# Kernel tuning notes

Hardware: AMD Instinct MI355X
Metric: run time of the kernel (lower is better)

## Reference

```python
import jax, jax.numpy as jnp
import numpy as np

B = 32           # graphs in batch
N_PER = 512      # nodes per graph
N = B * N_PER    # 16384 total nodes (block-diagonal batched graph)
E = N * 16       # 262144 edges
D_IN = 128
D_OUT = 128
ASSIGN = 2048    # total clusters = B * K
K = ASSIGN // B  # 64 clusters per graph


def setup_inputs() -> dict:
    key = jax.random.key(0)
    ks = jax.random.split(key, 6)
    h = jax.random.normal(ks[0], (N, D_IN), jnp.float32)
    # edges confined within each graph -> block-diagonal batched adjacency
    gid = jnp.repeat(jnp.arange(B), E // B)
    edge_src = (jax.random.randint(ks[1], (E,), 0, N_PER) + gid * N_PER).astype(jnp.int32)
    edge_dst = (jax.random.randint(ks[2], (E,), 0, N_PER) + gid * N_PER).astype(jnp.int32)
    # GraphSage NodeApply linears: Linear(2*in, out)
    stdv_f = 1.0 / np.sqrt(2 * D_IN)
    W_feat = jax.random.uniform(ks[3], (2 * D_IN, D_OUT), jnp.float32, -stdv_f, stdv_f)
    b_feat = jnp.zeros((D_OUT,), jnp.float32)
    W_pool = jax.random.uniform(ks[4], (2 * D_IN, ASSIGN), jnp.float32, -stdv_f, stdv_f)
    b_pool = jnp.zeros((ASSIGN,), jnp.float32)
    return {"h": h, "W_feat": W_feat, "b_feat": b_feat,
            "W_pool": W_pool, "b_pool": b_pool,
            "edge_src": edge_src, "edge_dst": edge_dst}


def _graphsage(h, W, b, src, dst):
    # mean aggregation over in-neighbors (dropout=0, batch_norm off)
    msg = jax.ops.segment_sum(h[src], dst, num_segments=N)          # [N, d_in]
    deg = jax.ops.segment_sum(jnp.ones((src.shape[0],), h.dtype), dst, num_segments=N)
    h_neigh = msg / jnp.maximum(deg, 1.0)[:, None]
    bundle = jnp.concatenate([h, h_neigh], axis=1) @ W + b          # [N, d_out]
    # F.normalize(p=2, dim=1) then activation, as in GraphSage NodeApply
    norm = jnp.linalg.norm(bundle, axis=1, keepdims=True)
    bundle = bundle / jnp.maximum(norm, 1e-12)
    return jax.nn.relu(bundle)


def _forward(h, W_feat, b_feat, W_pool, b_pool, src, dst):
    feat = _graphsage(h, W_feat, b_feat, src, dst)       # [N, D_OUT]
    assign = _graphsage(h, W_pool, b_pool, src, dst)     # [N, ASSIGN]
    # block-diagonal mask: node i of graph g may only assign to g's K clusters
    gid_n = jnp.arange(N) // N_PER                       # [N]
    gid_c = jnp.arange(ASSIGN) // K                      # [ASSIGN]
    mask = (gid_n[:, None] == gid_c[None, :]).astype(jnp.float32)
    # masked_softmax with memory_efficient=False
    s = jax.nn.softmax(assign * mask, axis=-1) * mask
    s = s / (s.sum(axis=-1, keepdims=True) + 1e-13)      # [N, ASSIGN]
    h_new = s.T @ feat                                   # [ASSIGN, D_OUT]
    # adj_new = S^T A S without densifying A: (A S)[dst] += S[src]
    a_s = jax.ops.segment_sum(s[src], dst, num_segments=N)
    adj_new = s.T @ a_s                                  # [ASSIGN, ASSIGN]
    return adj_new, h_new


def reference(h, W_feat, b_feat, W_pool, b_pool, edge_src, edge_dst):
    return _forward(h, W_feat, b_feat, W_pool, b_pool, edge_src, edge_dst)
```

## Files before the change

### kernel.cpp

```cpp
#include <hip/hip_runtime.h>

#define NB   32
#define NPER 512
#define NN   16384
#define EE   262144
#define DD   128
#define AS   2048
#define KC   64

using short8   = __attribute__((ext_vector_type(8))) short;
using floatx4  = __attribute__((ext_vector_type(4))) float;
using ushort4v = __attribute__((ext_vector_type(4))) unsigned short;

typedef __attribute__((address_space(3))) unsigned int lds_u32;
typedef const __attribute__((address_space(1))) unsigned int gbl_u32;

static __device__ __forceinline__ void gload16(const unsigned short* g, unsigned short* l) {
    __builtin_amdgcn_global_load_lds((gbl_u32*)g, (lds_u32*)l, 16, 0, 0);
}

static __device__ __forceinline__ float bits2f(unsigned int u) {
    union { unsigned int i; float f; } z; z.i = u << 16; return z.f;
}
static __device__ __forceinline__ unsigned short f2b(float x) {
    union { float f; unsigned int u; } v; v.f = x;
    unsigned int r = v.u + 0x7fffu + ((v.u >> 16) & 1u);
    return (unsigned short)(r >> 16);
}

__global__ void prep_kernel(const float* __restrict__ h, unsigned short* __restrict__ bundle,
                            unsigned short* __restrict__ hT, const int* __restrict__ esrc,
                            const int* __restrict__ edst, unsigned int* __restrict__ Acnt) {
    __shared__ unsigned short fT[128 * 136];
    int b = blockIdx.x, t = threadIdx.x;
    if (b < 128) {
        int node0 = b * 128;
        int r = t >> 1, hf = t & 1;
        const float4* h4 = reinterpret_cast<const float4*>(h + (size_t)(node0 + r) * 128 + hf * 64);
        unsigned short* bo = bundle + (size_t)(node0 + r) * 256 + hf * 64;
#pragma unroll
        for (int i = 0; i < 16; i++) {
            float4 v = h4[i];
            ushort4v o = { f2b(v.x), f2b(v.y), f2b(v.z), f2b(v.w) };
            *reinterpret_cast<ushort4v*>(bo + 4 * i) = o;
            int c = hf * 64 + 4 * i;
            fT[(c + 0) * 136 + r] = o.x;
            fT[(c + 1) * 136 + r] = o.y;
            fT[(c + 2) * 136 + r] = o.z;
            fT[(c + 3) * 136 + r] = o.w;
        }
        __syncthreads();
        int c = t >> 1, nh = t & 1;
        const uint4* src = reinterpret_cast<const uint4*>(&fT[c * 136 + nh * 64]);
        uint4* dst = reinterpret_cast<uint4*>(hT + (size_t)c * NN + node0 + nh * 64);
#pragma unroll
        for (int i = 0; i < 8; i++) dst[i] = src[i];
    } else {
        int e = (b - 128) * 256 + t;
        int d = edst[e], sl = esrc[e] & 511;
        int idx = d * 512 + sl;
        atomicAdd(&Acnt[idx >> 2], 1u << (8 * (idx & 3)));
    }
}

__global__ void conv_kernel(const unsigned int* __restrict__ Acnt,
                            unsigned short* __restrict__ Aadj, float* __restrict__ invdeg) {
    int t = threadIdx.x;
    int row = blockIdx.x * 8 + (t >> 5);
    int u = t & 31;
    uint4 w = reinterpret_cast<const uint4*>(Acnt)[(size_t)row * 32 + u];
    unsigned int wa[4] = { w.x, w.y, w.z, w.w };
    unsigned short out[16];
    float sum = 0.f;
#pragma unroll
    for (int i = 0; i < 4; i++) {
#pragma unroll
        for (int bb = 0; bb < 4; bb++) {
            float fv = (float)((wa[i] >> (8 * bb)) & 0xffu);
            sum += fv;
            out[4 * i + bb] = f2b(fv);
        }
    }
    unsigned int pw[8];
#pragma unroll
    for (int i = 0; i < 8; i++)
        pw[i] = (unsigned int)out[2 * i] | ((unsigned int)out[2 * i + 1] << 16);
    uint4* dst = reinterpret_cast<uint4*>(Aadj + (size_t)row * 512 + u * 16);
    uint4 s0 = { pw[0], pw[1], pw[2], pw[3] }, s1 = { pw[4], pw[5], pw[6], pw[7] };
    dst[0] = s0; dst[1] = s1;
#pragma unroll
    for (int d = 1; d < 32; d <<= 1) sum += __shfl_xor(sum, d, 64);
    if (u == 0) invdeg[row] = 1.0f / fmaxf(sum, 1.0f);
}

__global__ void transpose_cast2_kernel(const float* __restrict__ Wf, const float* __restrict__ Wp,
                                       unsigned short* __restrict__ WfT, unsigned short* __restrict__ WpT) {
    __shared__ float tl[32][33];
    int tx = threadIdx.x, ty = threadIdx.y;
    int bx = blockIdx.x;
    const float* in; unsigned short* out; int C, cb;
    if (bx < DD / 32) { in = Wf; out = WfT; C = DD; cb = bx; }
    else              { in = Wp; out = WpT; C = AS; cb = bx - DD / 32; }
    int c0 = cb * 32, r0 = blockIdx.y * 32;
    for (int i = 0; i < 4; i++)
        tl[ty + 8 * i][tx] = in[(size_t)(r0 + ty + 8 * i) * C + c0 + tx];
    __syncthreads();
    for (int i = 0; i < 4; i++)
        out[(size_t)(c0 + ty + 8 * i) * 256 + r0 + tx] = f2b(tl[tx][ty + 8 * i]);
}

__global__ __launch_bounds__(256) void agg_h_mfma_kernel(
    const unsigned short* __restrict__ Aadj, const unsigned short* __restrict__ hT,
    const float* __restrict__ invdeg, unsigned short* __restrict__ bundle) {
    __shared__ alignas(16) unsigned short lA[64 * 512];
    int tid = threadIdx.x, bx = blockIdx.x;
    int r0 = bx * 64, g = bx >> 3;
    int wv = tid >> 6, lane = tid & 63, q = lane >> 4, lm = lane & 15;
    int mw = wv >> 1, nw = wv & 1;
#pragma unroll
    for (int j = 0; j < 16; j++) {
        int u = tid + 256 * j;
        int row = u >> 6, cu = (u & 63) ^ (row & 7);
        gload16(Aadj + (size_t)(r0 + row) * 512 + cu * 8, &lA[u * 8]);
    }
    floatx4 acc[2][4];
#pragma unroll
    for (int mt = 0; mt < 2; mt++)
#pragma unroll
        for (int nt = 0; nt < 4; nt++) acc[mt][nt] = (floatx4)0.f;
    __syncthreads();

    const unsigned short* Bb = hT + (size_t)(64 * nw + lm) * NN + g * 512 + (q << 3);
    short8 bF[2][4];
#pragma unroll
    for (int nt = 0; nt < 4; nt++)
        bF[0][nt] = *reinterpret_cast<const short8*>(Bb + (size_t)16 * nt * NN);
    for (int ki = 0; ki < 16; ki++) {
        if (ki < 15) {
#pragma unroll
            for (int nt = 0; nt < 4; nt++)
                bF[(ki + 1) & 1][nt] =
                    *reinterpret_cast<const short8*>(Bb + (size_t)16 * nt * NN + (ki + 1) * 32);
        }
        short8 aF[2];
        int swz = (4 * ki + q) ^ (lm & 7);
#pragma unroll
        for (int mt = 0; mt < 2; mt++)
            aF[mt] = *reinterpret_cast<const short8*>(&lA[((32 * mw + 16 * mt + lm) * 64 + swz) * 8]);
#pragma unroll
        for (int mt = 0; mt < 2; mt++)
#pragma unroll
            for (int nt = 0; nt < 4; nt++)
                acc[mt][nt] = __builtin_amdgcn_mfma_f32_16x16x32_bf16(aF[mt], bF[ki & 1][nt],
                                                                      acc[mt][nt], 0, 0, 0);
    }
#pragma unroll
    for (int mt = 0; mt < 2; mt++)
#pragma unroll
        for (int r = 0; r < 4; r++) {
            int row = 32 * mw + 16 * mt + 4 * q + r;
            float inv = invdeg[r0 + row];
#pragma unroll
            for (int nt = 0; nt < 4; nt++)
                bundle[(size_t)(r0 + row) * 256 + 128 + 64 * nw + 16 * nt + lm] =
                    f2b(acc[mt][nt][r] * inv);
        }
}

__global__ __launch_bounds__(256) void feat_mfma_kernel(
    const unsigned short* __restrict__ bundle, const unsigned short* __restrict__ WfT,
    const float* __restrict__ bfe, unsigned short* __restrict__ featT) {
    __shared__ alignas(16) unsigned short lA[512 * 8];
    __shared__ alignas(16) unsigned short lB[512 * 8];
    __shared__ float red[256];
    __shared__ alignas(16) unsigned short fT[128 * 136];
    int tid = threadIdx.x;
    int r0 = blockIdx.x * 128;
    int wv = tid >> 6, lane = tid & 63;
    int mw = wv >> 1, nw = wv & 1, q = lane >> 4, lm = lane & 15;
    int rowS0 = tid >> 2,         cS0 = (tid & 3) ^ ((rowS0 >> 1) & 3);
    int rowS1 = (tid + 256) >> 2, cS1 = ((tid + 256) & 3) ^ ((rowS1 >> 1) & 3);
    int swz = q ^ ((lm >> 1) & 3);

    floatx4 acc[4][4];
#pragma unroll
    for (int mi = 0; mi < 4; mi++)
#pragma unroll
        for (int ni = 0; ni < 4; ni++) acc[mi][ni] = (floatx4)0.f;

    for (int k0 = 0; k0 < 256; k0 += 32) {
        gload16(bundle + (size_t)(r0 + rowS0) * 256 + k0 + 8 * cS0, &lA[tid * 8]);
        gload16(bundle + (size_t)(r0 + rowS1) * 256 + k0 + 8 * cS1, &lA[(tid + 256) * 8]);
        gload16(WfT + (size_t)rowS0 * 256 + k0 + 8 * cS0, &lB[tid * 8]);
        gload16(WfT + (size_t)rowS1 * 256 + k0 + 8 * cS1, &lB[(tid + 256) * 8]);
        __syncthreads();
        short8 aF[4], bF[4];
#pragma unroll
        for (int mi = 0; mi < 4; mi++)
            aF[mi] = *reinterpret_cast<const short8*>(&lA[((64 * mw + 16 * mi + lm) * 4 + swz) * 8]);
#pragma unroll
        for (int ni = 0; ni < 4; ni++)
            bF[ni] = *reinterpret_cast<const short8*>(&lB[((64 * nw + 16 * ni + lm) * 4 + swz) * 8]);
#pragma unroll
        for (int mi = 0; mi < 4; mi++)
#pragma unroll
            for (int ni = 0; ni < 4; ni++)
                acc[mi][ni] = __builtin_amdgcn_mfma_f32_16x16x32_bf16(aF[mi], bF[ni], acc[mi][ni], 0, 0, 0);
        __syncthreads();
    }
#pragma unroll
    for (int ni = 0; ni < 4; ni++) {
        float bv = bfe[64 * nw + 16 * ni + lm];
#pragma unroll
        for (int mi = 0; mi < 4; mi++)
#pragma unroll
            for (int r = 0; r < 4; r++) acc[mi][ni][r] += bv;
    }
#pragma unroll
    for (int mi = 0; mi < 4; mi++)
#pragma unroll
        for (int r = 0; r < 4; r++) {
            float p = 0.f;
#pragma unroll
            for (int ni = 0; ni < 4; ni++) p += acc[mi][ni][r] * acc[mi][ni][r];
            p += __shfl_xor(p, 1, 64);
            p += __shfl_xor(p, 2, 64);
            p += __shfl_xor(p, 4, 64);
            p += __shfl_xor(p, 8, 64);
            if (lm == 0) red[nw * 128 + 64 * mw + 16 * mi + 4 * q + r] = p;
        }
    __syncthreads();
#pragma unroll
    for (int mi = 0; mi < 4; mi++) {
        float rrn[4];
#pragma unroll
        for (int r = 0; r < 4; r++) {
            int rl = 64 * mw + 16 * mi + 4 * q + r;
            rrn[r] = 1.0f / fmaxf(sqrtf(red[rl] + red[128 + rl]), 1e-12f);
        }
#pragma unroll
        for (int ni = 0; ni < 4; ni++) {
            int col = 64 * nw + 16 * ni + lm;
            ushort4v pk = { f2b(fmaxf(acc[mi][ni][0] * rrn[0], 0.f)),
                            f2b(fmaxf(acc[mi][ni][1] * rrn[1], 0.f)),
                            f2b(fmaxf(acc[mi][ni][2] * rrn[2], 0.f)),
                            f2b(fmaxf(acc[mi][ni][3] * rrn[3], 0.f)) };
            *reinterpret_cast<ushort4v*>(&fT[col * 136 + 64 * mw + 16 * mi + 4 * q]) = pk;
        }
    }
    __syncthreads();
    {
        int col = tid >> 1, half = tid & 1;
        const uint4* src = reinterpret_cast<const uint4*>(&fT[col * 136 + half * 64]);
        uint4* dst = reinterpret_cast<uint4*>(featT + (size_t)col * NN + r0 + half * 64);
#pragma unroll
        for (int i = 0; i < 8; i++) dst[i] = src[i];
    }
}

__global__ __launch_bounds__(256) void pool_fused_kernel(
    const unsigned short* __restrict__ bundle, const unsigned short* __restrict__ WpT,
    const float* __restrict__ bp, unsigned short* __restrict__ sT) {
    __shared__ alignas(16) unsigned short lA[2048 * 8];
    __shared__ float raw[64 * 68];
    __shared__ float ssq_l[4 * 64];
    __shared__ float rn_l[64];
    int tid = threadIdx.x, bx = blockIdx.x;
    int r0 = bx * 64, g = bx >> 3;
    int wv = tid >> 6, lane = tid & 63, q = lane >> 4, lm = lane & 15;

#pragma unroll
    for (int j = 0; j < 8; j++) {
        int u = tid + 256 * j;
        int row = u >> 5;
        int chunk = (u & 31) ^ (row & 7);
        gload16(bundle + (size_t)(r0 + row) * 256 + chunk * 8, &lA[u * 8]);
    }
    float ssqacc[4][4];
#pragma unroll
    for (int mi = 0; mi < 4; mi++)
#pragma unroll
        for (int r = 0; r < 4; r++) ssqacc[mi][r] = 0.f;
    __syncthreads();

    for (int nc8 = 0; nc8 < 8; nc8++) {
        int nc = 4 * nc8 + wv;
        const unsigned short* Bb = WpT + ((size_t)(nc * 64 + lm) << 8) + (q << 3);
        short8 bF[2][4];
#pragma unroll
        for (int ni = 0; ni < 4; ni++)
            bF[0][ni] = *reinterpret_cast<const short8*>(Bb + (ni << 12));
        floatx4 acc[4][4];
#pragma unroll
        for (int mi = 0; mi < 4; mi++)
#pragma unroll
            for (int ni = 0; ni < 4; ni++) acc[mi][ni] = (floatx4)0.f;
#pragma unroll
        for (int k = 0; k < 8; k++) {
            if (k < 7) {
#pragma unroll
                for (int ni = 0; ni < 4; ni++)
                    bF[(k + 1) & 1][ni] =
                        *reinterpret_cast<const short8*>(Bb + (ni << 12) + ((k + 1) << 5));
            }
            short8 aF[4];
            int swz = (4 * k + q) ^ (lm & 7);
#pragma unroll
            for (int mi = 0; mi < 4; mi++)
                aF[mi] = *reinterpret_cast<const short8*>(&lA[((16 * mi + lm) * 32 + swz) * 8]);
#pragma unroll
            for (int mi = 0; mi < 4; mi++)
#pragma unroll
                for (int ni = 0; ni < 4; ni++)
                    acc[mi][ni] = __builtin_amdgcn_mfma_f32_16x16x32_bf16(aF[mi], bF[k & 1][ni],
                                                                          acc[mi][ni], 0, 0, 0);
        }
        float bv[4];
#pragma unroll
        for (int ni = 0; ni < 4; ni++) bv[ni] = bp[nc * 64 + 16 * ni + lm];
#pragma unroll
        for (int mi = 0; mi < 4; mi++)
#pragma unroll
            for (int r = 0; r < 4; r++) {
                float p = 0.f;
#pragma unroll
                for (int ni = 0; ni < 4; ni++) {
                    acc[mi][ni][r] += bv[ni];
                    p += acc[mi][ni][r] * acc[mi][ni][r];
                }
                ssqacc[mi][r] += p;
            }
        if (nc == g) {
#pragma unroll
            for (int mi = 0; mi < 4; mi++)
#pragma unroll
                for (int ni = 0; ni < 4; ni++)
#pragma unroll
                    for (int r = 0; r < 4; r++)
                        raw[(16 * mi + 4 * q + r) * 68 + 16 * ni + lm] = acc[mi][ni][r];
        }
    }
#pragma unroll
    for (int mi = 0; mi < 4; mi++)
#pragma unroll
        for (int r = 0; r < 4; r++) {
            float p = ssqacc[mi][r];
            p += __shfl_xor(p, 1, 64);
            p += __shfl_xor(p, 2, 64);
            p += __shfl_xor(p, 4, 64);
            p += __shfl_xor(p, 8, 64);
            if (lm == 0) ssq_l[wv * 64 + 16 * mi + 4 * q + r] = p;
        }
    __syncthreads();
    if (tid < 64)
        rn_l[tid] = 1.0f / fmaxf(sqrtf(ssq_l[tid] + ssq_l[64 + tid] + ssq_l[128 + tid] +
                                       ssq_l[192 + tid]), 1e-12f);
    __syncthreads();
    {
        int row = tid >> 2, j = tid & 3;
        int nloc = ((bx & 7) << 6) + row;
        float rn = rn_l[row];
        float v[16];
        float mx = -1e30f;
#pragma unroll
        for (int c4 = 0; c4 < 4; c4++) {
            float4 rv = *reinterpret_cast<const float4*>(&raw[row * 68 + 16 * j + 4 * c4]);
            v[4 * c4 + 0] = fmaxf(rv.x * rn, 0.f);
            v[4 * c4 + 1] = fmaxf(rv.y * rn, 0.f);
            v[4 * c4 + 2] = fmaxf(rv.z * rn, 0.f);
            v[4 * c4 + 3] = fmaxf(rv.w * rn, 0.f);
        }
#pragma unroll
        for (int c = 0; c < 16; c++) mx = fmaxf(mx, v[c]);
        mx = fmaxf(mx, __shfl_xor(mx, 1, 64));
        mx = fmaxf(mx, __shfl_xor(mx, 2, 64));
        float z = 0.f;
#pragma unroll
        for (int c = 0; c < 16; c++) { v[c] = __expf(v[c] - mx); z += v[c]; }
        z += __shfl_xor(z, 1, 64);
        z += __shfl_xor(z, 2, 64);
        float iz = 1.0f / z;
#pragma unroll
        for (int c4 = 0; c4 < 4; c4++) {
            size_t tb = (size_t)(g * KC + 16 * j + 4 * c4) * NPER + nloc;
            sT[tb] = f2b(v[4 * c4 + 0] * iz);
            sT[tb + NPER] = f2b(v[4 * c4 + 1] * iz);
            sT[tb + 2 * NPER] = f2b(v[4 * c4 + 2] * iz);
            sT[tb + 3 * NPER] = f2b(v[4 * c4 + 3] * iz);
        }
    }
}

__global__ __launch_bounds__(256) void as_mfma_kernel(
    const unsigned short* __restrict__ sT, const unsigned short* __restrict__ Aadj,
    unsigned short* __restrict__ asT) {
    __shared__ alignas(16) unsigned short lS[64 * 512];
    int tid = threadIdx.x, bx = blockIdx.x;
    int g = bx >> 1, half = bx & 1;
    int wv = tid >> 6, lane = tid & 63, q = lane >> 4, lm = lane & 15;
#pragma unroll
    for (int j = 0; j < 16; j++) {
        int u = tid + 256 * j;
        int row = u >> 6, cu = (u & 63) ^ (row & 7);
        gload16(sT + (size_t)(g * KC + row) * NPER + cu * 8, &lS[u * 8]);
    }
    floatx4 acc[4][4];
#pragma unroll
    for (int mi = 0; mi < 4; mi++)
#pragma unroll
        for (int nt = 0; nt < 4; nt++) acc[mi][nt] = (floatx4)0.f;
    __syncthreads();

    int dbase = half * 256 + wv * 64;
    const unsigned short* Bb = Aadj + (size_t)(g * 512 + dbase + lm) * 512 + (q << 3);
    short8 bF[2][4];
#pragma unroll
    for (int nt = 0; nt < 4; nt++)
        bF[0][nt] = *reinterpret_cast<const short8*>(Bb + (size_t)16 * nt * 512);
    for (int ki = 0; ki < 16; ki++) {
        if (ki < 15) {
#pragma unroll
            for (int nt = 0; nt < 4; nt++)
                bF[(ki + 1) & 1][nt] =
                    *reinterpret_cast<const short8*>(Bb + (size_t)16 * nt * 512 + (ki + 1) * 32);
        }
        short8 aF[4];
        int swz = (4 * ki + q) ^ (lm & 7);
#pragma unroll
        for (int mi = 0; mi < 4; mi++)
            aF[mi] = *reinterpret_cast<const short8*>(&lS[((16 * mi + lm) * 64 + swz) * 8]);
#pragma unroll
        for (int mi = 0; mi < 4; mi++)
#pragma unroll
            for (int nt = 0; nt < 4; nt++)
                acc[mi][nt] = __builtin_amdgcn_mfma_f32_16x16x32_bf16(aF[mi], bF[ki & 1][nt],
                                                                      acc[mi][nt], 0, 0, 0);
    }
#pragma unroll
    for (int mi = 0; mi < 4; mi++)
#pragma unroll
        for (int r = 0; r < 4; r++) {
            int row = 16 * mi + 4 * q + r;
#pragma unroll
            for (int nt = 0; nt < 4; nt++)
                asT[(size_t)(g * KC + row) * NPER + dbase + 16 * nt + lm] = f2b(acc[mi][nt][r]);
        }
}

__global__ __launch_bounds__(256) void hnew_adj_kernel(
    const unsigned short* __restrict__ sT, const unsigned short* __restrict__ featT,
    const unsigned short* __restrict__ asT, float* __restrict__ adjf,
    float* __restrict__ hnewf) {
    __shared__ alignas(16) unsigned short lS[1024 * 8];
    __shared__ alignas(16) unsigned short lF[2048 * 8];
    __shared__ alignas(16) unsigned short lAS[1024 * 8];
    int tid = threadIdx.x;
    int ch = blockIdx.x, g = blockIdx.y;
    int k0 = g * NPER + ch * 128;
    int wv = tid >> 6, lane = tid & 63, q = lane >> 4, lm = lane & 15;

#pragma unroll
    for (int j = 0; j < 4; j++) {
        int u = tid + 256 * j;
        int row = u >> 4, cu = (u & 15) ^ (row & 15);
        gload16(sT + (size_t)(g * KC + row) * NPER + ch * 128 + cu * 8, &lS[u * 8]);
    }
#pragma unroll
    for (int j = 0; j < 8; j++) {
        int u = tid + 256 * j;
        int row = u >> 4, cu = (u & 15) ^ (row & 15);
        gload16(featT + (size_t)row * NN + k0 + cu * 8, &lF[u * 8]);
    }
#pragma unroll
    for (int j = 0; j < 4; j++) {
        int u = tid + 256 * j;
        int row = u >> 4, cu = (u & 15) ^ (row & 15);
        gload16(asT + (size_t)(g * KC + row) * NPER + ch * 128 + cu * 8, &lAS[u * 8]);
    }
    floatx4 acc[4][4];
#pragma unroll
    for (int mi = 0; mi < 4; mi++)
#pragma unroll
        for (int ni = 0; ni < 4; ni++) acc[mi][ni] = (floatx4)0.f;
    __syncthreads();

    bool isH = (wv < 2);
    for (int ks = 0; ks < 4; ks++) {
        if (!isH && (ks >> 1) != (wv & 1)) continue;
        short8 aF[4], bF[4];
#pragma unroll
        for (int mi = 0; mi < 4; mi++)
            aF[mi] = *reinterpret_cast<const short8*>(
                &lS[((16 * mi + lm) * 16 + ((4 * ks + q) ^ lm)) * 8]);
        if (isH) {
#pragma unroll
            for (int ni = 0; ni < 4; ni++)
                bF[ni] = *reinterpret_cast<const short8*>(
                    &lF[((64 * wv + 16 * ni + lm) * 16 + ((4 * ks + q) ^ lm)) * 8]);
        } else {
#pragma unroll
            for (int ni = 0; ni < 4; ni++)
                bF[ni] = *reinterpret_cast<const short8*>(
                    &lAS[((16 * ni + lm) * 16 + ((4 * ks + q) ^ lm)) * 8]);
        }
#pragma unroll
        for (int mi = 0; mi < 4; mi++)
#pragma unroll
            for (int ni = 0; ni < 4; ni++)
                acc[mi][ni] = __builtin_amdgcn_mfma_f32_16x16x32_bf16(aF[mi], bF[ni], acc[mi][ni], 0, 0, 0);
    }
    if (isH) {
#pragma unroll
        for (int mi = 0; mi < 4; mi++)
#pragma unroll
            for (int ni = 0; ni < 4; ni++)
#pragma unroll
                for (int r = 0; r < 4; r++)
                    atomicAdd(&hnewf[(size_t)(g * KC + 16 * mi + 4 * q + r) * DD +
                                     64 * wv + 16 * ni + lm], acc[mi][ni][r]);
    } else {
#pragma unroll
        for (int mi = 0; mi < 4; mi++)
#pragma unroll
            for (int ni = 0; ni < 4; ni++)
#pragma unroll
                for (int r = 0; r < 4; r++)
                    atomicAdd(&adjf[(size_t)(g * KC + 16 * mi + 4 * q + r) * AS +
                                    g * KC + 16 * ni + lm], acc[mi][ni][r]);
    }
}

extern "C" void kernel_launch(void* const* d_in, const int* in_sizes, int n_in,
                              void* d_out, int out_size, void* d_ws, size_t ws_size,
                              hipStream_t stream) {
    const float* h   = (const float*)d_in[0];
    const float* Wf  = (const float*)d_in[1];
    const float* bfe = (const float*)d_in[2];
    const float* Wp  = (const float*)d_in[3];
    const float* bp  = (const float*)d_in[4];
    const int* esrc  = (const int*)d_in[5];
    const int* edst  = (const int*)d_in[6];

    float* adjf  = (float*)d_out;
    float* hnewf = adjf + (size_t)AS * AS;

    unsigned short* bundle = (unsigned short*)d_ws;
    unsigned short* WfT   = bundle + (size_t)NN * 256;
    unsigned short* WpT   = WfT + 128 * 256;
    unsigned short* sT    = WpT + (size_t)AS * 256;
    unsigned short* asT   = sT + (size_t)NN * KC;
    unsigned short* featT = asT + (size_t)NN * KC;
    unsigned short* hT    = featT + (size_t)DD * NN;
    unsigned short* Aadj  = hT + (size_t)DD * NN;
    float* invdeg = (float*)(Aadj + (size_t)NN * 512);
    unsigned int* Acnt = (unsigned int*)(invdeg + NN);

    hipMemsetAsync(Acnt, 0, (size_t)NN * 512, stream);
    hipMemsetAsync(d_out, 0, ((size_t)AS * AS + (size_t)AS * DD) * sizeof(float), stream);

    prep_kernel<<<128 + EE / 256, 256, 0, stream>>>(h, bundle, hT, esrc, edst, Acnt);
    conv_kernel<<<NN / 8, 256, 0, stream>>>(Acnt, Aadj, invdeg);
    transpose_cast2_kernel<<<dim3(DD / 32 + AS / 32, 256 / 32), dim3(32, 8), 0, stream>>>(
        Wf, Wp, WfT, WpT);
    agg_h_mfma_kernel<<<NN / 64, 256, 0, stream>>>(Aadj, hT, invdeg, bundle);
    feat_mfma_kernel<<<NN / 128, 256, 0, stream>>>(bundle, WfT, bfe, featT);
    pool_fused_kernel<<<NN / 64, 256, 0, stream>>>(bundle, WpT, bp, sT);
    as_mfma_kernel<<<NB * 2, 256, 0, stream>>>(sT, Aadj, asT);
    hnew_adj_kernel<<<dim3(4, NB), 256, 0, stream>>>(sT, featT, asT, adjf, hnewf);
}
```

Before: 185.7 us.

## Merge weight transpose, feat/pool kernels, and replace output memset/atomics with direct stores

Folds the weight transpose-cast into the prep kernel as extra blocks and merges the feat and pool GEMM kernels into one launch that branches on block index. The final h_new/adj kernel now has one block per graph that loops over the 512 nodes in four chunks, so it writes its results with plain stores instead of atomics. Extra blocks zero the off-diagonal adjacency tiles, which replaces the full output memset. This cuts launches, memset traffic and atomic contention, but the final kernel has only 32 compute blocks, which lowers parallelism.

```diff
diff --git a/kernel.cpp b/kernel.cpp
--- a/kernel.cpp
+++ b/kernel.cpp
@@ -28,10 +28,16 @@
     return (unsigned short)(r >> 16);
 }
 
+union PrepSMem {
+    unsigned short fT[128 * 136];
+    float tl[32][33];
+};
 __global__ void prep_kernel(const float* __restrict__ h, unsigned short* __restrict__ bundle,
                             unsigned short* __restrict__ hT, const int* __restrict__ esrc,
-                            const int* __restrict__ edst, unsigned int* __restrict__ Acnt) {
-    __shared__ unsigned short fT[128 * 136];
+                            const int* __restrict__ edst, unsigned int* __restrict__ Acnt,
+                            const float* __restrict__ Wf, const float* __restrict__ Wp,
+                            unsigned short* __restrict__ WfT, unsigned short* __restrict__ WpT) {
+    __shared__ PrepSMem sm;
     int b = blockIdx.x, t = threadIdx.x;
     if (b < 128) {
         int node0 = b * 128;
@@ -44,22 +50,35 @@
             ushort4v o = { f2b(v.x), f2b(v.y), f2b(v.z), f2b(v.w) };
             *reinterpret_cast<ushort4v*>(bo + 4 * i) = o;
             int c = hf * 64 + 4 * i;
-            fT[(c + 0) * 136 + r] = o.x;
-            fT[(c + 1) * 136 + r] = o.y;
-            fT[(c + 2) * 136 + r] = o.z;
-            fT[(c + 3) * 136 + r] = o.w;
+            sm.fT[(c + 0) * 136 + r] = o.x;
+            sm.fT[(c + 1) * 136 + r] = o.y;
+            sm.fT[(c + 2) * 136 + r] = o.z;
+            sm.fT[(c + 3) * 136 + r] = o.w;
         }
         __syncthreads();
         int c = t >> 1, nh = t & 1;
-        const uint4* src = reinterpret_cast<const uint4*>(&fT[c * 136 + nh * 64]);
+        const uint4* src = reinterpret_cast<const uint4*>(&sm.fT[c * 136 + nh * 64]);
         uint4* dst = reinterpret_cast<uint4*>(hT + (size_t)c * NN + node0 + nh * 64);
 #pragma unroll
         for (int i = 0; i < 8; i++) dst[i] = src[i];
-    } else {
+    } else if (b < 1152) {
         int e = (b - 128) * 256 + t;
         int d = edst[e], sl = esrc[e] & 511;
         int idx = d * 512 + sl;
         atomicAdd(&Acnt[idx >> 2], 1u << (8 * (idx & 3)));
+    } else {
+        int tb = b - 1152;
+        int bx = tb % 68, by = tb / 68;
+        int tx = t & 31, ty = t >> 5;
+        const float* in; unsigned short* out; int C, cb;
+        if (bx < DD / 32) { in = Wf; out = WfT; C = DD; cb = bx; }
+        else              { in = Wp; out = WpT; C = AS; cb = bx - DD / 32; }
+        int c0 = cb * 32, r0 = by * 32;
+        for (int i = 0; i < 4; i++)
+            sm.tl[ty + 8 * i][tx] = in[(size_t)(r0 + ty + 8 * i) * C + c0 + tx];
+        __syncthreads();
+        for (int i = 0; i < 4; i++)
+            out[(size_t)(c0 + ty + 8 * i) * 256 + r0 + tx] = f2b(sm.tl[tx][ty + 8 * i]);
     }
 }
 
@@ -93,22 +112,6 @@
     if (u == 0) invdeg[row] = 1.0f / fmaxf(sum, 1.0f);
 }
 
-__global__ void transpose_cast2_kernel(const float* __restrict__ Wf, const float* __restrict__ Wp,
-                                       unsigned short* __restrict__ WfT, unsigned short* __restrict__ WpT) {
-    __shared__ float tl[32][33];
-    int tx = threadIdx.x, ty = threadIdx.y;
-    int bx = blockIdx.x;
-    const float* in; unsigned short* out; int C, cb;
-    if (bx < DD / 32) { in = Wf; out = WfT; C = DD; cb = bx; }
-    else              { in = Wp; out = WpT; C = AS; cb = bx - DD / 32; }
-    int c0 = cb * 32, r0 = blockIdx.y * 32;
-    for (int i = 0; i < 4; i++)
-        tl[ty + 8 * i][tx] = in[(size_t)(r0 + ty + 8 * i) * C + c0 + tx];
-    __syncthreads();
-    for (int i = 0; i < 4; i++)
-        out[(size_t)(c0 + ty + 8 * i) * 256 + r0 + tx] = f2b(tl[tx][ty + 8 * i]);
-}
-
 __global__ __launch_bounds__(256) void agg_h_mfma_kernel(
     const unsigned short* __restrict__ Aadj, const unsigned short* __restrict__ hT,
     const float* __restrict__ invdeg, unsigned short* __restrict__ bundle) {
@@ -129,7 +132,6 @@
 #pragma unroll
         for (int nt = 0; nt < 4; nt++) acc[mt][nt] = (floatx4)0.f;
     __syncthreads();
-
     const unsigned short* Bb = hT + (size_t)(64 * nw + lm) * NN + g * 512 + (q << 3);
     short8 bF[2][4];
 #pragma unroll
@@ -167,226 +169,220 @@
         }
 }
 
-__global__ __launch_bounds__(256) void feat_mfma_kernel(
+union FPSMem {
+    struct { unsigned short lA[4096]; unsigned short lB[4096]; float red[256];
+             unsigned short fT[17408]; } feat;
+    struct { unsigned short lA[16384]; float raw[4352]; float ssq[256]; float rn[64]; } pool;
+};
+__global__ __launch_bounds__(256) void featpool_kernel(
     const unsigned short* __restrict__ bundle, const unsigned short* __restrict__ WfT,
-    const float* __restrict__ bfe, unsigned short* __restrict__ featT) {
-    __shared__ alignas(16) unsigned short lA[512 * 8];
-    __shared__ alignas(16) unsigned short lB[512 * 8];
-    __shared__ float red[256];
-    __shared__ alignas(16) unsigned short fT[128 * 136];
-    int tid = threadIdx.x;
-    int r0 = blockIdx.x * 128;
-    int wv = tid >> 6, lane = tid & 63;
-    int mw = wv >> 1, nw = wv & 1, q = lane >> 4, lm = lane & 15;
-    int rowS0 = tid >> 2,         cS0 = (tid & 3) ^ ((rowS0 >> 1) & 3);
-    int rowS1 = (tid + 256) >> 2, cS1 = ((tid + 256) & 3) ^ ((rowS1 >> 1) & 3);
-    int swz = q ^ ((lm >> 1) & 3);
-
-    floatx4 acc[4][4];
-#pragma unroll
-    for (int mi = 0; mi < 4; mi++)
-#pragma unroll
-        for (int ni = 0; ni < 4; ni++) acc[mi][ni] = (floatx4)0.f;
-
-    for (int k0 = 0; k0 < 256; k0 += 32) {
-        gload16(bundle + (size_t)(r0 + rowS0) * 256 + k0 + 8 * cS0, &lA[tid * 8]);
-        gload16(bundle + (size_t)(r0 + rowS1) * 256 + k0 + 8 * cS1, &lA[(tid + 256) * 8]);
-        gload16(WfT + (size_t)rowS0 * 256 + k0 + 8 * cS0, &lB[tid * 8]);
-        gload16(WfT + (size_t)rowS1 * 256 + k0 + 8 * cS1, &lB[(tid + 256) * 8]);
-        __syncthreads();
-        short8 aF[4], bF[4];
-#pragma unroll
-        for (int mi = 0; mi < 4; mi++)
-            aF[mi] = *reinterpret_cast<const short8*>(&lA[((64 * mw + 16 * mi + lm) * 4 + swz) * 8]);
-#pragma unroll
-        for (int ni = 0; ni < 4; ni++)
-            bF[ni] = *reinterpret_cast<const short8*>(&lB[((64 * nw + 16 * ni + lm) * 4 + swz) * 8]);
-#pragma unroll
-        for (int mi = 0; mi < 4; mi++)
+    const unsigned short* __restrict__ WpT, const float* __restrict__ bfe,
+    const float* __restrict__ bp, unsigned short* __restrict__ featT,
+    unsigned short* __restrict__ sT) {
+    __shared__ FPSMem sm;
+    int tid = threadIdx.x, b = blockIdx.x;
+    if (b < 128) {
+        int r0 = b * 128;
+        int wv = tid >> 6, lane = tid & 63;
+        int mw = wv >> 1, nw = wv & 1, q = lane >> 4, lm = lane & 15;
+        int rowS0 = tid >> 2,         cS0 = (tid & 3) ^ ((rowS0 >> 1) & 3);
+        int rowS1 = (tid + 256) >> 2, cS1 = ((tid + 256) & 3) ^ ((rowS1 >> 1) & 3);
+        int swz = q ^ ((lm >> 1) & 3);
+        floatx4 acc[4][4];
+#pragma unroll
+        for (int mi = 0; mi < 4; mi++)
+#pragma unroll
+            for (int ni = 0; ni < 4; ni++) acc[mi][ni] = (floatx4)0.f;
+        for (int k0 = 0; k0 < 256; k0 += 32) {
+            gload16(bundle + (size_t)(r0 + rowS0) * 256 + k0 + 8 * cS0, &sm.feat.lA[tid * 8]);
+            gload16(bundle + (size_t)(r0 + rowS1) * 256 + k0 + 8 * cS1, &sm.feat.lA[(tid + 256) * 8]);
+            gload16(WfT + (size_t)rowS0 * 256 + k0 + 8 * cS0, &sm.feat.lB[tid * 8]);
+            gload16(WfT + (size_t)rowS1 * 256 + k0 + 8 * cS1, &sm.feat.lB[(tid + 256) * 8]);
+            __syncthreads();
+            short8 aF[4], bF[4];
+#pragma unroll
+            for (int mi = 0; mi < 4; mi++)
+                aF[mi] = *reinterpret_cast<const short8*>(&sm.feat.lA[((64 * mw + 16 * mi + lm) * 4 + swz) * 8]);
 #pragma unroll
             for (int ni = 0; ni < 4; ni++)
-                acc[mi][ni] = __builtin_amdgcn_mfma_f32_16x16x32_bf16(aF[mi], bF[ni], acc[mi][ni], 0, 0, 0);
-        __syncthreads();
-    }
-#pragma unroll
-    for (int ni = 0; ni < 4; ni++) {
-        float bv = bfe[64 * nw + 16 * ni + lm];
-#pragma unroll
-        for (int mi = 0; mi < 4; mi++)
-#pragma unroll
-            for (int r = 0; r < 4; r++) acc[mi][ni][r] += bv;
-    }
-#pragma unroll
-    for (int mi = 0; mi < 4; mi++)
-#pragma unroll
-        for (int r = 0; r < 4; r++) {
-            float p = 0.f;
-#pragma unroll
-            for (int ni = 0; ni < 4; ni++) p += acc[mi][ni][r] * acc[mi][ni][r];
-            p += __shfl_xor(p, 1, 64);
-            p += __shfl_xor(p, 2, 64);
-            p += __shfl_xor(p, 4, 64);
-            p += __shfl_xor(p, 8, 64);
-            if (lm == 0) red[nw * 128 + 64 * mw + 16 * mi + 4 * q + r] = p;
-        }
-    __syncthreads();
-#pragma unroll
-    for (int mi = 0; mi < 4; mi++) {
-        float rrn[4];
-#pragma unroll
-        for (int r = 0; r < 4; r++) {
-            int rl = 64 * mw + 16 * mi + 4 * q + r;
-            rrn[r] = 1.0f / fmaxf(sqrtf(red[rl] + red[128 + rl]), 1e-12f);
+                bF[ni] = *reinterpret_cast<const short8*>(&sm.feat.lB[((64 * nw + 16 * ni + lm) * 4 + swz) * 8]);
+#pragma unroll
+            for (int mi = 0; mi < 4; mi++)
+#pragma unroll
+                for (int ni = 0; ni < 4; ni++)
+                    acc[mi][ni] = __builtin_amdgcn_mfma_f32_16x16x32_bf16(aF[mi], bF[ni], acc[mi][ni], 0, 0, 0);
+            __syncthreads();
         }
 #pragma unroll
         for (int ni = 0; ni < 4; ni++) {
-            int col = 64 * nw + 16 * ni + lm;
-            ushort4v pk = { f2b(fmaxf(acc[mi][ni][0] * rrn[0], 0.f)),
-                            f2b(fmaxf(acc[mi][ni][1] * rrn[1], 0.f)),
-                            f2b(fmaxf(acc[mi][ni][2] * rrn[2], 0.f)),
-                            f2b(fmaxf(acc[mi][ni][3] * rrn[3], 0.f)) };
-            *reinterpret_cast<ushort4v*>(&fT[col * 136 + 64 * mw + 16 * mi + 4 * q]) = pk;
-        }
-    }
-    __syncthreads();
-    {
-        int col = tid >> 1, half = tid & 1;
-        const uint4* src = reinterpret_cast<const uint4*>(&fT[col * 136 + half * 64]);
-        uint4* dst = reinterpret_cast<uint4*>(featT + (size_t)col * NN + r0 + half * 64);
-#pragma unroll
-        for (int i = 0; i < 8; i++) dst[i] = src[i];
-    }
-}
-
-__global__ __launch_bounds__(256) void pool_fused_kernel(
-    const unsigned short* __restrict__ bundle, const unsigned short* __restrict__ WpT,
-    const float* __restrict__ bp, unsigned short* __restrict__ sT) {
-    __shared__ alignas(16) unsigned short lA[2048 * 8];
-    __shared__ float raw[64 * 68];
-    __shared__ float ssq_l[4 * 64];
-    __shared__ float rn_l[64];
-    int tid = threadIdx.x, bx = blockIdx.x;
-    int r0 = bx * 64, g = bx >> 3;
-    int wv = tid >> 6, lane = tid & 63, q = lane >> 4, lm = lane & 15;
-
-#pragma unroll
-    for (int j = 0; j < 8; j++) {
-        int u = tid + 256 * j;
-        int row = u >> 5;
-        int chunk = (u & 31) ^ (row & 7);
-        gload16(bundle + (size_t)(r0 + row) * 256 + chunk * 8, &lA[u * 8]);
-    }
-    float ssqacc[4][4];
-#pragma unroll
-    for (int mi = 0; mi < 4; mi++)
-#pragma unroll
-        for (int r = 0; r < 4; r++) ssqacc[mi][r] = 0.f;
-    __syncthreads();
-
-    for (int nc8 = 0; nc8 < 8; nc8++) {
-        int nc = 4 * nc8 + wv;
-        const unsigned short* Bb = WpT + ((size_t)(nc * 64 + lm) << 8) + (q << 3);
-        short8 bF[2][4];
-#pragma unroll
-        for (int ni = 0; ni < 4; ni++)
-            bF[0][ni] = *reinterpret_cast<const short8*>(Bb + (ni << 12));
-        floatx4 acc[4][4];
-#pragma unroll
-        for (int mi = 0; mi < 4; mi++)
-#pragma unroll
-            for (int ni = 0; ni < 4; ni++) acc[mi][ni] = (floatx4)0.f;
-#pragma unroll
-        for (int k = 0; k < 8; k++) {
-            if (k < 7) {
-#pragma unroll
-                for (int ni = 0; ni < 4; ni++)
-                    bF[(k + 1) & 1][ni] =
-                        *reinterpret_cast<const short8*>(Bb + (ni << 12) + ((k + 1) << 5));
-            }
-            short8 aF[4];
-            int swz = (4 * k + q) ^ (lm & 7);
+            float bv = bfe[64 * nw + 16 * ni + lm];
 #pragma unroll
             for (int mi = 0; mi < 4; mi++)
-                aF[mi] = *reinterpret_cast<const short8*>(&lA[((16 * mi + lm) * 32 + swz) * 8]);
-#pragma unroll
-            for (int mi = 0; mi < 4; mi++)
-#pragma unroll
-                for (int ni = 0; ni < 4; ni++)
-                    acc[mi][ni] = __builtin_amdgcn_mfma_f32_16x16x32_bf16(aF[mi], bF[k & 1][ni],
-                                                                          acc[mi][ni], 0, 0, 0);
-        }
-        float bv[4];
-#pragma unroll
-        for (int ni = 0; ni < 4; ni++) bv[ni] = bp[nc * 64 + 16 * ni + lm];
+#pragma unroll
+                for (int r = 0; r < 4; r++) acc[mi][ni][r] += bv;
+        }
 #pragma unroll
         for (int mi = 0; mi < 4; mi++)
 #pragma unroll
             for (int r = 0; r < 4; r++) {
                 float p = 0.f;
 #pragma unroll
-                for (int ni = 0; ni < 4; ni++) {
-                    acc[mi][ni][r] += bv[ni];
-                    p += acc[mi][ni][r] * acc[mi][ni][r];
+                for (int ni = 0; ni < 4; ni++) p += acc[mi][ni][r] * acc[mi][ni][r];
+                p += __shfl_xor(p, 1, 64);
+                p += __shfl_xor(p, 2, 64);
+                p += __shfl_xor(p, 4, 64);
+                p += __shfl_xor(p, 8, 64);
+                if (lm == 0) sm.feat.red[nw * 128 + 64 * mw + 16 * mi + 4 * q + r] = p;
+            }
+        __syncthreads();
+#pragma unroll
+        for (int mi = 0; mi < 4; mi++) {
+            float rrn[4];
+#pragma unroll
+            for (int r = 0; r < 4; r++) {
+                int rl = 64 * mw + 16 * mi + 4 * q + r;
+                rrn[r] = 1.0f / fmaxf(sqrtf(sm.feat.red[rl] + sm.feat.red[128 + rl]), 1e-12f);
+            }
+#pragma unroll
+            for (int ni = 0; ni < 4; ni++) {
+                int col = 64 * nw + 16 * ni + lm;
+                ushort4v pk = { f2b(fmaxf(acc[mi][ni][0] * rrn[0], 0.f)),
+                                f2b(fmaxf(acc[mi][ni][1] * rrn[1], 0.f)),
+                                f2b(fmaxf(acc[mi][ni][2] * rrn[2], 0.f)),
+                                f2b(fmaxf(acc[mi][ni][3] * rrn[3], 0.f)) };
+                *reinterpret_cast<ushort4v*>(&sm.feat.fT[col * 136 + 64 * mw + 16 * mi + 4 * q]) = pk;
+            }
+        }
+        __syncthreads();
+        {
+            int col = tid >> 1, half = tid & 1;
+            const uint4* src = reinterpret_cast<const uint4*>(&sm.feat.fT[col * 136 + half * 64]);
+            uint4* dst = reinterpret_cast<uint4*>(featT + (size_t)col * NN + r0 + half * 64);
+#pragma unroll
+            for (int i = 0; i < 8; i++) dst[i] = src[i];
+        }
+    } else {
+        int bx = b - 128;
+        int r0 = bx * 64, g = bx >> 3;
+        int wv = tid >> 6, lane = tid & 63, q = lane >> 4, lm = lane & 15;
+#pragma unroll
+        for (int j = 0; j < 8; j++) {
+            int u = tid + 256 * j;
+            int row = u >> 5;
+            int chunk = (u & 31) ^ (row & 7);
+            gload16(bundle + (size_t)(r0 + row) * 256 + chunk * 8, &sm.pool.lA[u * 8]);
+        }
+        float ssqacc[4][4];
+#pragma unroll
+        for (int mi = 0; mi < 4; mi++)
+#pragma unroll
+            for (int r = 0; r < 4; r++) ssqacc[mi][r] = 0.f;
+        __syncthreads();
+        for (int nc8 = 0; nc8 < 8; nc8++) {
+            int nc = 4 * nc8 + wv;
+            const unsigned short* Bb = WpT + ((size_t)(nc * 64 + lm) << 8) + (q << 3);
+            short8 bF[2][4];
+#pragma unroll
+            for (int ni = 0; ni < 4; ni++)
+                bF[0][ni] = *reinterpret_cast<const short8*>(Bb + (ni << 12));
+            floatx4 acc[4][4];
+#pragma unroll
+            for (int mi = 0; mi < 4; mi++)
+#pragma unroll
+                for (int ni = 0; ni < 4; ni++) acc[mi][ni] = (floatx4)0.f;
+#pragma unroll
+            for (int k = 0; k < 8; k++) {
+                if (k < 7) {
+#pragma unroll
+                    for (int ni = 0; ni < 4; ni++)
+                        bF[(k + 1) & 1][ni] =
+                            *reinterpret_cast<const short8*>(Bb + (ni << 12) + ((k + 1) << 5));
                 }
-                ssqacc[mi][r] += p;
-            }
-        if (nc == g) {
+                short8 aF[4];
+                int swz = (4 * k + q) ^ (lm & 7);
+#pragma unroll
+                for (int mi = 0; mi < 4; mi++)
+                    aF[mi] = *reinterpret_cast<const short8*>(&sm.pool.lA[((16 * mi + lm) * 32 + swz) * 8]);
+#pragma unroll
+                for (int mi = 0; mi < 4; mi++)
+#pragma unroll
+                    for (int ni = 0; ni < 4; ni++)
+                        acc[mi][ni] = __builtin_amdgcn_mfma_f32_16x16x32_bf16(aF[mi], bF[k & 1][ni],
+                                                                              acc[mi][ni], 0, 0, 0);
+            }
+            float bv[4];
+#pragma unroll
+            for (int ni = 0; ni < 4; ni++) bv[ni] = bp[nc * 64 + 16 * ni + lm];
 #pragma unroll
             for (int mi = 0; mi < 4; mi++)
 #pragma unroll
-                for (int ni = 0; ni < 4; ni++)
-#pragma unroll
-                    for (int r = 0; r < 4; r++)
-                        raw[(16 * mi + 4 * q + r) * 68 + 16 * ni + lm] = acc[mi][ni][r];
-        }
-    }
-#pragma unroll
-    for (int mi = 0; mi < 4; mi++)
-#pragma unroll
-        for (int r = 0; r < 4; r++) {
-            float p = ssqacc[mi][r];
-            p += __shfl_xor(p, 1, 64);
-            p += __shfl_xor(p, 2, 64);
-            p += __shfl_xor(p, 4, 64);
-            p += __shfl_xor(p, 8, 64);
-            if (lm == 0) ssq_l[wv * 64 + 16 * mi + 4 * q + r] = p;
-        }
-    __syncthreads();
-    if (tid < 64)
-        rn_l[tid] = 1.0f / fmaxf(sqrtf(ssq_l[tid] + ssq_l[64 + tid] + ssq_l[128 + tid] +
-                                       ssq_l[192 + tid]), 1e-12f);
-    __syncthreads();
-    {
-        int row = tid >> 2, j = tid & 3;
-        int nloc = ((bx & 7) << 6) + row;
-        float rn = rn_l[row];
-        float v[16];
-        float mx = -1e30f;
-#pragma unroll
-        for (int c4 = 0; c4 < 4; c4++) {
-            float4 rv = *reinterpret_cast<const float4*>(&raw[row * 68 + 16 * j + 4 * c4]);
-            v[4 * c4 + 0] = fmaxf(rv.x * rn, 0.f);
-            v[4 * c4 + 1] = fmaxf(rv.y * rn, 0.f);
-            v[4 * c4 + 2] = fmaxf(rv.z * rn, 0.f);
-            v[4 * c4 + 3] = fmaxf(rv.w * rn, 0.f);
-        }
-#pragma unroll
-        for (int c = 0; c < 16; c++) mx = fmaxf(mx, v[c]);
-        mx = fmaxf(mx, __shfl_xor(mx, 1, 64));
-        mx = fmaxf(mx, __shfl_xor(mx, 2, 64));
-        float z = 0.f;
-#pragma unroll
-        for (int c = 0; c < 16; c++) { v[c] = __expf(v[c] - mx); z += v[c]; }
-        z += __shfl_xor(z, 1, 64);
-        z += __shfl_xor(z, 2, 64);
-        float iz = 1.0f / z;
-#pragma unroll
-        for (int c4 = 0; c4 < 4; c4++) {
-            size_t tb = (size_t)(g * KC + 16 * j + 4 * c4) * NPER + nloc;
-            sT[tb] = f2b(v[4 * c4 + 0] * iz);
-            sT[tb + NPER] = f2b(v[4 * c4 + 1] * iz);
-            sT[tb + 2 * NPER] = f2b(v[4 * c4 + 2] * iz);
-            sT[tb + 3 * NPER] = f2b(v[4 * c4 + 3] * iz);
+                for (int r = 0; r < 4; r++) {
+                    float p = 0.f;
+#pragma unroll
+                    for (int ni = 0; ni < 4; ni++) {
+                        acc[mi][ni][r] += bv[ni];
+                        p += acc[mi][ni][r] * acc[mi][ni][r];
+                    }
+                    ssqacc[mi][r] += p;
+                }
+            if (nc == g) {
+#pragma unroll
+                for (int mi = 0; mi < 4; mi++)
+#pragma unroll
+                    for (int ni = 0; ni < 4; ni++)
+#pragma unroll
+                        for (int r = 0; r < 4; r++)
+                            sm.pool.raw[(16 * mi + 4 * q + r) * 68 + 16 * ni + lm] = acc[mi][ni][r];
+            }
+        }
+#pragma unroll
+        for (int mi = 0; mi < 4; mi++)
+#pragma unroll
+            for (int r = 0; r < 4; r++) {
+                float p = ssqacc[mi][r];
+                p += __shfl_xor(p, 1, 64);
+                p += __shfl_xor(p, 2, 64);
+                p += __shfl_xor(p, 4, 64);
+                p += __shfl_xor(p, 8, 64);
+                if (lm == 0) sm.pool.ssq[wv * 64 + 16 * mi + 4 * q + r] = p;
+            }
+        __syncthreads();
+        if (tid < 64)
+            sm.pool.rn[tid] = 1.0f / fmaxf(sqrtf(sm.pool.ssq[tid] + sm.pool.ssq[64 + tid] +
+                                           sm.pool.ssq[128 + tid] + sm.pool.ssq[192 + tid]), 1e-12f);
+        __syncthreads();
+        {
+            int row = tid >> 2, j = tid & 3;
+            int nloc = ((bx & 7) << 6) + row;
+            float rn = sm.pool.rn[row];
+            float v[16];
+            float mx = -1e30f;
+#pragma unroll
+            for (int c4 = 0; c4 < 4; c4++) {
+                float4 rv = *reinterpret_cast<const float4*>(&sm.pool.raw[row * 68 + 16 * j + 4 * c4]);
+                v[4 * c4 + 0] = fmaxf(rv.x * rn, 0.f);
+                v[4 * c4 + 1] = fmaxf(rv.y * rn, 0.f);
+                v[4 * c4 + 2] = fmaxf(rv.z * rn, 0.f);
+                v[4 * c4 + 3] = fmaxf(rv.w * rn, 0.f);
+            }
+#pragma unroll
+            for (int c = 0; c < 16; c++) mx = fmaxf(mx, v[c]);
+            mx = fmaxf(mx, __shfl_xor(mx, 1, 64));
+            mx = fmaxf(mx, __shfl_xor(mx, 2, 64));
+            float z = 0.f;
+#pragma unroll
+            for (int c = 0; c < 16; c++) { v[c] = __expf(v[c] - mx); z += v[c]; }
+            z += __shfl_xor(z, 1, 64);
+            z += __shfl_xor(z, 2, 64);
+            float iz = 1.0f / z;
+#pragma unroll
+            for (int c4 = 0; c4 < 4; c4++) {
+                size_t tb = (size_t)(g * KC + 16 * j + 4 * c4) * NPER + nloc;
+                sT[tb] = f2b(v[4 * c4 + 0] * iz);
+                sT[tb + NPER] = f2b(v[4 * c4 + 1] * iz);
+                sT[tb + 2 * NPER] = f2b(v[4 * c4 + 2] * iz);
+                sT[tb + 3 * NPER] = f2b(v[4 * c4 + 3] * iz);
+            }
         }
     }
 }
@@ -410,7 +406,6 @@
 #pragma unroll
         for (int nt = 0; nt < 4; nt++) acc[mi][nt] = (floatx4)0.f;
     __syncthreads();
-
     int dbase = half * 256 + wv * 64;
     const unsigned short* Bb = Aadj + (size_t)(g * 512 + dbase + lm) * 512 + (q << 3);
     short8 bF[2][4];
@@ -447,86 +442,109 @@
         }
 }
 
-__global__ __launch_bounds__(256) void hnew_adj_kernel(
+__global__ __launch_bounds__(256) void hnew_adj2_kernel(
     const unsigned short* __restrict__ sT, const unsigned short* __restrict__ featT,
     const unsigned short* __restrict__ asT, float* __restrict__ adjf,
     float* __restrict__ hnewf) {
     __shared__ alignas(16) unsigned short lS[1024 * 8];
     __shared__ alignas(16) unsigned short lF[2048 * 8];
     __shared__ alignas(16) unsigned short lAS[1024 * 8];
-    int tid = threadIdx.x;
-    int ch = blockIdx.x, g = blockIdx.y;
-    int k0 = g * NPER + ch * 128;
+    int tid = threadIdx.x, b = blockIdx.x;
+    if (b >= 32) {
+        uint4 z = { 0u, 0u, 0u, 0u };
+        for (int row = b - 32; row < AS; row += 224) {
+            int g = row >> 6;
+            uint4* out = reinterpret_cast<uint4*>(adjf + (size_t)row * AS);
+            for (int i = tid; i < 512; i += 256)
+                if (i < g * 16 || i >= g * 16 + 16) out[i] = z;
+        }
+        return;
+    }
+    int g = b;
     int wv = tid >> 6, lane = tid & 63, q = lane >> 4, lm = lane & 15;
-
-#pragma unroll
-    for (int j = 0; j < 4; j++) {
-        int u = tid + 256 * j;
-        int row = u >> 4, cu = (u & 15) ^ (row & 15);
-        gload16(sT + (size_t)(g * KC + row) * NPER + ch * 128 + cu * 8, &lS[u * 8]);
-    }
-#pragma unroll
-    for (int j = 0; j < 8; j++) {
-        int u = tid + 256 * j;
-        int row = u >> 4, cu = (u & 15) ^ (row & 15);
-        gload16(featT + (size_t)row * NN + k0 + cu * 8, &lF[u * 8]);
-    }
-#pragma unroll
-    for (int j = 0; j < 4; j++) {
-        int u = tid + 256 * j;
-        int row = u >> 4, cu = (u & 15) ^ (row & 15);
-        gload16(asT + (size_t)(g * KC + row) * NPER + ch * 128 + cu * 8, &lAS[u * 8]);
-    }
-    floatx4 acc[4][4];
-#pragma unroll
-    for (int mi = 0; mi < 4; mi++)
-#pragma unroll
-        for (int ni = 0; ni < 4; ni++) acc[mi][ni] = (floatx4)0.f;
-    __syncthreads();
-
     bool isH = (wv < 2);
+    floatx4 accH[4][4];
+    floatx4 accA[4][2];
+#pragma unroll
+    for (int mi = 0; mi < 4; mi++) {
+#pragma unroll
+        for (int ni = 0; ni < 4; ni++) accH[mi][ni] = (floatx4)0.f;
+#pragma unroll
+        for (int ni = 0; ni < 2; ni++) accA[mi][ni] = (floatx4)0.f;
+    }
     for (int ks = 0; ks < 4; ks++) {
-        if (!isH && (ks >> 1) != (wv & 1)) continue;
-        short8 aF[4], bF[4];
-#pragma unroll
-        for (int mi = 0; mi < 4; mi++)
-            aF[mi] = *reinterpret_cast<const short8*>(
-                &lS[((16 * mi + lm) * 16 + ((4 * ks + q) ^ lm)) * 8]);
-        if (isH) {
+#pragma unroll
+        for (int j = 0; j < 4; j++) {
+            int u = tid + 256 * j;
+            int row = u >> 4, cu = (u & 15) ^ (row & 15);
+            gload16(sT + (size_t)(g * KC + row) * NPER + ks * 128 + cu * 8, &lS[u * 8]);
+        }
+#pragma unroll
+        for (int j = 0; j < 8; j++) {
+            int u = tid + 256 * j;
+            int row = u >> 4, cu = (u & 15) ^ (row & 15);
+            gload16(featT + (size_t)row * NN + g * NPER + ks * 128 + cu * 8, &lF[u * 8]);
+        }
+#pragma unroll
+        for (int j = 0; j < 4; j++) {
+            int u = tid + 256 * j;
+            int row = u >> 4, cu = (u & 15) ^ (row & 15);
+            gload16(asT + (size_t)(g * KC + row) * NPER + ks * 128 + cu * 8, &lAS[u * 8]);
+        }
+        __syncthreads();
+#pragma unroll
+        for (int kk = 0; kk < 4; kk++) {
+            short8 aF[4];
+#pragma unroll
+            for (int mi = 0; mi < 4; mi++)
+                aF[mi] = *reinterpret_cast<const short8*>(
+                    &lS[((16 * mi + lm) * 16 + ((4 * kk + q) ^ lm)) * 8]);
+            if (isH) {
+                short8 bF[4];
+#pragma unroll
+                for (int ni = 0; ni < 4; ni++)
+                    bF[ni] = *reinterpret_cast<const short8*>(
+                        &lF[((64 * wv + 16 * ni + lm) * 16 + ((4 * kk + q) ^ lm)) * 8]);
+#pragma unroll
+                for (int mi = 0; mi < 4; mi++)
+#pragma unroll
+                    for (int ni = 0; ni < 4; ni++)
+                        accH[mi][ni] = __builtin_amdgcn_mfma_f32_16x16x32_bf16(aF[mi], bF[ni],
+                                                                               accH[mi][ni], 0, 0, 0);
+            } else {
+                short8 bF[2];
+#pragma unroll
+                for (int ni = 0; ni < 2; ni++)
+                    bF[ni] = *reinterpret_cast<const short8*>(
+                        &lAS[((32 * (wv - 2) + 16 * ni + lm) * 16 + ((4 * kk + q) ^ lm)) * 8]);
+#pragma unroll
+                for (int mi = 0; mi < 4; mi++)
+#pragma unroll
+                    for (int ni = 0; ni < 2; ni++)
+                        accA[mi][ni] = __builtin_amdgcn_mfma_f32_16x16x32_bf16(aF[mi], bF[ni],
+                                                                               accA[mi][ni], 0, 0, 0);
+            }
+        }
+        __syncthreads();
+    }
+    if (isH) {
+#pragma unroll
+        for (int mi = 0; mi < 4; mi++)
 #pragma unroll
             for (int ni = 0; ni < 4; ni++)
-                bF[ni] = *reinterpret_cast<const short8*>(
-                    &lF[((64 * wv + 16 * ni + lm) * 16 + ((4 * ks + q) ^ lm)) * 8]);
-        } else {
-#pragma unroll
-            for (int ni = 0; ni < 4; ni++)
-                bF[ni] = *reinterpret_cast<const short8*>(
-                    &lAS[((16 * ni + lm) * 16 + ((4 * ks + q) ^ lm)) * 8]);
-        }
-#pragma unroll
-        for (int mi = 0; mi < 4; mi++)
-#pragma unroll
-            for (int ni = 0; ni < 4; ni++)
-                acc[mi][ni] = __builtin_amdgcn_mfma_f32_16x16x32_bf16(aF[mi], bF[ni], acc[mi][ni], 0, 0, 0);
-    }
-    if (isH) {
-#pragma unroll
-        for (int mi = 0; mi < 4; mi++)
-#pragma unroll
-            for (int ni = 0; ni < 4; ni++)
 #pragma unroll
                 for (int r = 0; r < 4; r++)
-                    atomicAdd(&hnewf[(size_t)(g * KC + 16 * mi + 4 * q + r) * DD +
-                                     64 * wv + 16 * ni + lm], acc[mi][ni][r]);
+                    hnewf[(size_t)(g * KC + 16 * mi + 4 * q + r) * DD +
+                          64 * wv + 16 * ni + lm] = accH[mi][ni][r];
     } else {
 #pragma unroll
         for (int mi = 0; mi < 4; mi++)
 #pragma unroll
-            for (int ni = 0; ni < 4; ni++)
+            for (int ni = 0; ni < 2; ni++)
 #pragma unroll
                 for (int r = 0; r < 4; r++)
-                    atomicAdd(&adjf[(size_t)(g * KC + 16 * mi + 4 * q + r) * AS +
-                                    g * KC + 16 * ni + lm], acc[mi][ni][r]);
+                    adjf[(size_t)(g * KC + 16 * mi + 4 * q + r) * AS +
+                         g * KC + 32 * (wv - 2) + 16 * ni + lm] = accA[mi][ni][r];
     }
 }
 
@@ -556,15 +574,12 @@
     unsigned int* Acnt = (unsigned int*)(invdeg + NN);
 
     hipMemsetAsync(Acnt, 0, (size_t)NN * 512, stream);
-    hipMemsetAsync(d_out, 0, ((size_t)AS * AS + (size_t)AS * DD) * sizeof(float), stream);
-
-    prep_kernel<<<128 + EE / 256, 256, 0, stream>>>(h, bundle, hT, esrc, edst, Acnt);
+
+    prep_kernel<<<128 + EE / 256 + 544, 256, 0, stream>>>(h, bundle, hT, esrc, edst, Acnt,
+                                                          Wf, Wp, WfT, WpT);
     conv_kernel<<<NN / 8, 256, 0, stream>>>(Acnt, Aadj, invdeg);
-    transpose_cast2_kernel<<<dim3(DD / 32 + AS / 32, 256 / 32), dim3(32, 8), 0, stream>>>(
-        Wf, Wp, WfT, WpT);
     agg_h_mfma_kernel<<<NN / 64, 256, 0, stream>>>(Aadj, hT, invdeg, bundle);
-    feat_mfma_kernel<<<NN / 128, 256, 0, stream>>>(bundle, WfT, bfe, featT);
-    pool_fused_kernel<<<NN / 64, 256, 0, stream>>>(bundle, WpT, bp, sT);
+    featpool_kernel<<<384, 256, 0, stream>>>(bundle, WfT, WpT, bfe, bp, featT, sT);
     as_mfma_kernel<<<NB * 2, 256, 0, stream>>>(sT, Aadj, asT);
-    hnew_adj_kernel<<<dim3(4, NB), 256, 0, stream>>>(sT, featT, asT, adjf, hnewf);
-}
+    hnew_adj2_kernel<<<256, 256, 0, stream>>>(sT, featT, asT, adjf, hnewf);
+}
```

Measured after the change: 181.2 us. 1.03x faster.
